# Performance work log

Hardware: AMD Instinct MI355X
Metric: run time of the kernel (lower is better)

## Reference

```python
import jax, jax.numpy as jnp
import numpy as np

NUM_EMBED = 1024
NUM_HEADS = 16
BLOCK_SIZE = 2048


def setup_inputs() -> dict:
    key = jax.random.key(0)
    k1, k2, k3, k4, k5 = jax.random.split(key, 5)
    C = NUM_EMBED
    s = 1.0 / np.sqrt(C)
    x = jax.random.normal(k1, (2, BLOCK_SIZE, C), dtype=jnp.float32)
    # nn.Linear params: weight (out,in), bias (out,)
    w_attn = jax.random.uniform(k2, (3 * C, C), minval=-s, maxval=s, dtype=jnp.float32)
    b_attn = jax.random.uniform(k3, (3 * C,), minval=-s, maxval=s, dtype=jnp.float32)
    w_proj = jax.random.uniform(k4, (C, C), minval=-s, maxval=s, dtype=jnp.float32)
    b_proj = jax.random.uniform(k5, (C,), minval=-s, maxval=s, dtype=jnp.float32)
    return {"x": x, "w_attn": w_attn, "b_attn": b_attn, "w_proj": w_proj, "b_proj": b_proj}


def reference(x, w_attn, b_attn, w_proj, b_proj):
    B, T, C = x.shape
    H = NUM_HEADS
    D = C // H
    kqv = jnp.einsum('btc,oc->bto', x, w_attn) + b_attn  # (B,T,3C)
    # Original code splits as K, Q, V in that order.
    K, Q, V = jnp.split(kqv, 3, axis=2)
    K = K.reshape(B, T, H, D).transpose(0, 2, 1, 3)  # (B,H,T,D)
    Q = Q.reshape(B, T, H, D).transpose(0, 2, 1, 3)
    V = V.reshape(B, T, H, D).transpose(0, 2, 1, 3)
    aff = jnp.einsum('bhqd,bhkd->bhqk', Q, K) * (D ** -0.5)  # (B,H,T,T)
    causal = jnp.tril(jnp.ones((T, T), dtype=bool))
    aff = jnp.where(causal[None, None], aff, jnp.float32(-jnp.inf))
    wei = jax.nn.softmax(aff, axis=-1)
    attn = jnp.einsum('bhqk,bhkd->bhqd', wei, V)
    attn = attn.transpose(0, 2, 1, 3).reshape(B, T, C)
    out = jnp.einsum('btc,oc->bto', attn, w_proj) + b_proj
    return out
```

## Files before the change

### kernel.cpp

```cpp
#include <hip/hip_runtime.h>
#include <hip/hip_bf16.h>
#include <cstdint>

typedef __attribute__((ext_vector_type(8))) short bf16x8;
typedef __attribute__((ext_vector_type(4))) float f32x4;
typedef __attribute__((ext_vector_type(16))) float f32x16;
typedef __attribute__((ext_vector_type(4))) uint16_t u16x4;

__device__ __forceinline__ uint16_t f2b(float f) {
  union { float f; uint32_t i; } v; v.f = f;
  return (uint16_t)((v.i + 0x7FFFu + ((v.i >> 16) & 1u)) >> 16);
}

__device__ __forceinline__ uint32_t pkbf(float a, float b) {
  union { __hip_bfloat162 h2; uint32_t u; } c;
  c.h2 = __float22bfloat162_rn(make_float2(a, b));
  return c.u;
}

#define GLDS16(g, l) __builtin_amdgcn_global_load_lds( \
    (const __attribute__((address_space(1))) void*)(g), \
    (__attribute__((address_space(3))) void*)(l), 16, 0, 0)

__global__ __launch_bounds__(256) void cvt_all(
    const float* __restrict__ x, const float* __restrict__ wa, const float* __restrict__ wp,
    uint16_t* __restrict__ xb, uint16_t* __restrict__ wab, uint16_t* __restrict__ wpb) {
  const int i = (blockIdx.x * 256 + threadIdx.x) * 4;
  const float* src; uint16_t* dst; int off;
  if (i < 4194304)      { src = x;  dst = xb;  off = i; }
  else if (i < 7340032) { src = wa; dst = wab; off = i - 4194304; }
  else                  { src = wp; dst = wpb; off = i - 7340032; }
  const float4 v = *(const float4*)(src + off);
  u16x4 o;
  o.x = f2b(v.x); o.y = f2b(v.y); o.z = f2b(v.z); o.w = f2b(v.w);
  *(u16x4*)(dst + off) = o;
}

template <int BM, bool OUT_BF16>
__global__ __launch_bounds__(256) void gemm_bt_bias(
    const uint16_t* __restrict__ A, const uint16_t* __restrict__ B,
    const float* __restrict__ bias, void* __restrict__ Cv,
    int M, int N, int K) {
  constexpr int MI = BM / 32;
  constexpr int CA = BM / 16;
  constexpr int CPW = (2 * (CA + 8)) / 4;
  constexpr int CT_PITCH = OUT_BF16 ? 72 : 68;
  constexpr size_t CT_BYTES = (size_t)4 * (BM / 2) * CT_PITCH * (OUT_BF16 ? 2 : 4);
  constexpr size_t ST_BYTES = (size_t)(2 * (BM * 32 + 4096)) * 2;
  constexpr size_t LB = CT_BYTES > ST_BYTES ? CT_BYTES : ST_BYTES;
  __shared__ alignas(16) unsigned char ldsb[LB];
  uint16_t* lds = (uint16_t*)ldsb;
  const int offB0 = BM * 32;
  const int offA1 = BM * 32 + 4096;
  const int offB1 = 2 * BM * 32 + 4096;

  const int tid = threadIdx.x;
  const int wave = tid >> 6, lane = tid & 63;
  const int q4 = lane >> 4, l16 = lane & 15;
  const int wm = wave >> 1, wn = wave & 1;
  const long blockM = (long)blockIdx.y * BM;
  const long blockN = (long)blockIdx.x * 128;

  f32x4 acc[MI][4] = {};

  for (int k0 = 0; k0 < K; k0 += 64) {
#pragma unroll
    for (int c = 0; c < CPW; ++c) {
      const int id = c * 4 + wave;
      const uint16_t* mat; long rowBase; int a, kk, off;
      if (id < CA)               { mat = A; rowBase = blockM; a = id;            kk = k0;      off = 0; }
      else if (id < CA + 8)      { mat = B; rowBase = blockN; a = id - CA;       kk = k0;      off = offB0; }
      else if (id < 2 * CA + 8)  { mat = A; rowBase = blockM; a = id - CA - 8;   kk = k0 + 32; off = offA1; }
      else                       { mat = B; rowBase = blockN; a = id - 2*CA - 8; kk = k0 + 32; off = offB1; }
      const int flat = a * 64 + lane;
      const int row = flat >> 2, seg = flat & 3;
      GLDS16(mat + (rowBase + row) * (long)K + kk + seg * 8, lds + off + a * 512);
    }
    __syncthreads();
#pragma unroll
    for (int h = 0; h < 2; ++h) {
      const uint16_t* Ah = lds + (h ? offA1 : 0);
      const uint16_t* Bh = lds + (h ? offB1 : offB0);
      bf16x8 af[MI], bfr[4];
#pragma unroll
      for (int i = 0; i < MI; ++i)
        af[i] = *(const bf16x8*)&Ah[(wm * (BM / 2) + i * 16 + l16) * 32 + q4 * 8];
#pragma unroll
      for (int j = 0; j < 4; ++j)
        bfr[j] = *(const bf16x8*)&Bh[(wn * 64 + j * 16 + l16) * 32 + q4 * 8];
#pragma unroll
      for (int i = 0; i < MI; ++i)
#pragma unroll
        for (int j = 0; j < 4; ++j)
          acc[i][j] = __builtin_amdgcn_mfma_f32_16x16x32_bf16(af[i], bfr[j], acc[i][j], 0, 0, 0);
    }
    __syncthreads();
  }

  if (OUT_BF16) {
    uint16_t* ct = lds + wave * (BM / 2) * 72;
#pragma unroll
    for (int j = 0; j < 4; ++j) {
      const float bv = bias[blockN + wn * 64 + j * 16 + l16];
#pragma unroll
      for (int i = 0; i < MI; ++i)
#pragma unroll
        for (int r = 0; r < 4; ++r)
          ct[(i * 16 + q4 * 4 + r) * 72 + j * 16 + l16] = f2b(acc[i][j][r] + bv);
    }
    __syncthreads();
    uint16_t* Cb = (uint16_t*)Cv;
#pragma unroll
    for (int st = 0; st < BM / 16; ++st) {
      const int flat = st * 64 + lane;
      const int row = flat >> 3, seg = flat & 7;
      const bf16x8 v = *(const bf16x8*)&ct[row * 72 + seg * 8];
      *(bf16x8*)&Cb[(blockM + wm * (BM / 2) + row) * (long)N + blockN + wn * 64 + seg * 8] = v;
    }
  } else {
    float* ct = (float*)ldsb + wave * (BM / 2) * 68;
#pragma unroll
    for (int j = 0; j < 4; ++j) {
      const float bv = bias[blockN + wn * 64 + j * 16 + l16];
#pragma unroll
      for (int i = 0; i < MI; ++i)
#pragma unroll
        for (int r = 0; r < 4; ++r)
          ct[(i * 16 + q4 * 4 + r) * 68 + j * 16 + l16] = acc[i][j][r] + bv;
    }
    __syncthreads();
    float* Cb = (float*)Cv;
#pragma unroll
    for (int st = 0; st < BM / 8; ++st) {
      const int flat = st * 64 + lane;
      const int row = flat >> 4, seg = flat & 15;
      const f32x4 v = *(const f32x4*)&ct[row * 68 + seg * 4];
      *(f32x4*)&Cb[(blockM + wm * (BM / 2) + row) * (long)N + blockN + wn * 64 + seg * 4] = v;
    }
  }
}

__global__ __launch_bounds__(256, 2) void attn_flash(
    const uint16_t* __restrict__ kqv, uint16_t* __restrict__ attn) {
  constexpr int T = 2048, C = 1024, C3 = 3072;
  __shared__ alignas(16) unsigned char ldsb[35840];
  uint16_t* KP = (uint16_t*)ldsb;
  uint16_t* Vt = (uint16_t*)(ldsb + 18432);
  uint32_t* VtW = (uint32_t*)(ldsb + 18432);
  float* mlb  = (float*)ldsb;
  float* obuf = (float*)(ldsb + 1024);

  const int tid = threadIdx.x;
  const int wave = tid >> 6, lane = tid & 63;
  const int l32 = lane & 31, hh = lane >> 5;
  const int sidx = blockIdx.x >> 5, bh = blockIdx.x & 31;
  const int b = bh >> 4, h = bh & 15;
  const size_t base = (size_t)b * T * C3;
  const int hD = h * 64;
  const int qb = 31 - sidx;
  const int nkt = (qb >> 1) + 1;
  const int tr = tid >> 3, kch = tid & 7;
  const float sc = 0.125f * 1.4426950408889634f;

  bf16x8 qf[2][4];
#pragma unroll
  for (int qc = 0; qc < 2; ++qc)
#pragma unroll
    for (int m = 0; m < 4; ++m)
      qf[qc][m] = *(const bf16x8*)&kqv[base + (size_t)(qb * 64 + qc * 32 + l32) * C3 + C + hD + m * 16 + hh * 8];

  f32x16 o[2][2] = {};
  float m_i[2] = {-1e30f, -1e30f}, l_i[2] = {0.f, 0.f};

  bf16x8 pk[4], pv0[2], pv1[2];
#pragma unroll
  for (int rr = 0; rr < 4; ++rr)
    pk[rr] = *(const bf16x8*)&kqv[base + (size_t)(rr * 32 + tr) * C3 + hD + kch * 8];
#pragma unroll
  for (int s2 = 0; s2 < 2; ++s2) {
    const size_t gg = base + (size_t)(2 * (s2 * 32 + tr)) * C3 + 2 * C + hD + kch * 8;
    pv0[s2] = *(const bf16x8*)&kqv[gg];
    pv1[s2] = *(const bf16x8*)&kqv[gg + C3];
  }

  for (int kt = 0; kt < nkt; ++kt) {
    __syncthreads();
#pragma unroll
    for (int rr = 0; rr < 4; ++rr)
      *(bf16x8*)&KP[(rr * 32 + tr) * 72 + kch * 8] = pk[rr];
#pragma unroll
    for (int s2 = 0; s2 < 2; ++s2) {
      const int colw = ((s2 * 32 + tr) + 8 * kch) & 63;
      const uint32_t* a0 = (const uint32_t*)&pv0[s2];
      const uint32_t* a1 = (const uint32_t*)&pv1[s2];
#pragma unroll
      for (int i = 0; i < 8; ++i) {
        const uint32_t w = (i & 1)
            ? __builtin_amdgcn_perm(a1[i >> 1], a0[i >> 1], 0x07060302u)
            : __builtin_amdgcn_perm(a1[i >> 1], a0[i >> 1], 0x05040100u);
        VtW[(kch * 8 + i) * 68 + colw] = w;
      }
    }
    __syncthreads();
    if (kt + 1 < nkt) {
      const int kb2 = (kt + 1) * 128;
#pragma unroll
      for (int rr = 0; rr < 4; ++rr)
        pk[rr] = *(const bf16x8*)&kqv[base + (size_t)(kb2 + rr * 32 + tr) * C3 + hD + kch * 8];
#pragma unroll
      for (int s2 = 0; s2 < 2; ++s2) {
        const size_t gg = base + (size_t)(kb2 + 2 * (s2 * 32 + tr)) * C3 + 2 * C + hD + kch * 8;
        pv0[s2] = *(const bf16x8*)&kqv[gg];
        pv1[s2] = *(const bf16x8*)&kqv[gg + C3];
      }
    }

    const bool act = (kt * 128 + wave * 32) <= (qb * 64 + 63);
    if (act) {
      bf16x8 kf[4];
#pragma unroll
      for (int m = 0; m < 4; ++m)
        kf[m] = *(const bf16x8*)&KP[(wave * 32 + l32) * 72 + m * 16 + hh * 8];

#pragma unroll
      for (int qc = 0; qc < 2; ++qc) {
        f32x16 z = {};
#pragma unroll
        for (int m = 0; m < 4; ++m)
          z = __builtin_amdgcn_mfma_f32_32x32x16_bf16(kf[m], qf[qc][m], z, 0, 0, 0);
        if (kt == nkt - 1) {
          const int key0 = kt * 128 + wave * 32;
          const int qg = qb * 64 + qc * 32 + l32;
#pragma unroll
          for (int r = 0; r < 16; ++r) {
            const int kg = key0 + (r & 3) + 8 * (r >> 2) + 4 * hh;
            if (kg > qg) z[r] = -1e30f;
          }
        }
        float mloc = -1e30f;
#pragma unroll
        for (int r = 0; r < 16; ++r) mloc = fmaxf(mloc, z[r]);
        mloc = fmaxf(mloc, __shfl_xor(mloc, 32, 64));
        const float pm = fmaxf(mloc * sc, -3.0e4f);
        if (__any(pm - m_i[qc] > 8.0f)) {
          const float mnew = fmaxf(m_i[qc], pm);
          const float alpha = exp2f(m_i[qc] - mnew);
#pragma unroll
          for (int r = 0; r < 16; ++r) {
            const float ar = __shfl(alpha, (r & 3) + 8 * (r >> 2) + 4 * hh, 64);
            o[qc][0][r] *= ar;
            o[qc][1][r] *= ar;
          }
          l_i[qc] *= alpha;
          m_i[qc] = mnew;
        }
        float rs = 0.f;
#pragma unroll
        for (int r = 0; r < 16; ++r) {
          const float pe = exp2f(fmaf(z[r], sc, -m_i[qc]));
          z[r] = pe;
          rs += pe;
        }
        rs += __shfl_xor(rs, 32, 64);
        l_i[qc] += rs;

        uint32_t x0 = pkbf(z[0], z[1]),   x1 = pkbf(z[2], z[3]);
        uint32_t y0 = pkbf(z[4], z[5]),   y1 = pkbf(z[6], z[7]);
        uint32_t x2 = pkbf(z[8], z[9]),   x3 = pkbf(z[10], z[11]);
        uint32_t y2 = pkbf(z[12], z[13]), y3 = pkbf(z[14], z[15]);
        const uint32_t s0 = hh ? x0 : y0, s1 = hh ? x1 : y1;
        const uint32_t s2 = hh ? x2 : y2, s3 = hh ? x3 : y3;
        const uint32_t t0 = __shfl_xor(s0, 32, 64), t1 = __shfl_xor(s1, 32, 64);
        const uint32_t t2 = __shfl_xor(s2, 32, 64), t3 = __shfl_xor(s3, 32, 64);
#pragma unroll
        for (int cc = 0; cc < 2; ++cc) {
          union { bf16x8 v; uint32_t w[4]; } pa;
          if (cc == 0) {
            pa.w[0] = hh ? t0 : x0; pa.w[1] = hh ? t1 : x1;
            pa.w[2] = hh ? y0 : t0; pa.w[3] = hh ? y1 : t1;
          } else {
            pa.w[0] = hh ? t2 : x2; pa.w[1] = hh ? t3 : x3;
            pa.w[2] = hh ? y2 : t2; pa.w[3] = hh ? y3 : t3;
          }
#pragma unroll
          for (int db = 0; db < 2; ++db) {
            const int d = db * 32 + l32;
            const int col = (wave * 32 + cc * 16 + hh * 8 + 16 * (d >> 3)) & 127;
            const bf16x8 vf = *(const bf16x8*)&Vt[d * 136 + col];
            o[qc][db] = __builtin_amdgcn_mfma_f32_32x32x16_bf16(pa.v, vf, o[qc][db], 0, 0, 0);
          }
        }
      }
    }
  }

#pragma unroll
  for (int qc = 0; qc < 2; ++qc) {
    __syncthreads();
    if (hh == 0) {
      mlb[wave * 64 + l32] = m_i[qc];
      mlb[wave * 64 + 32 + l32] = l_i[qc];
    }
#pragma unroll
    for (int r = 0; r < 16; ++r) {
      const int ql = (r & 3) + 8 * (r >> 2) + 4 * hh;
      const int bw = wave * 2112 + ql * 66 + l32;
      obuf[bw] = o[qc][0][r];
      obuf[bw + 32] = o[qc][1][r];
    }
    __syncthreads();
    float mw[4], lw[4];
#pragma unroll
    for (int w = 0; w < 4; ++w) {
      mw[w] = mlb[w * 64 + l32];
      lw[w] = mlb[w * 64 + 32 + l32];
    }
    const float M = fmaxf(fmaxf(mw[0], mw[1]), fmaxf(mw[2], mw[3]));
    float L = 0.f, ww[4];
#pragma unroll
    for (int w = 0; w < 4; ++w) { ww[w] = exp2f(mw[w] - M); L += lw[w] * ww[w]; }
    const float Li = 1.0f / L;
    const int cb = wave * 2 + hh;
    float acc[8] = {};
#pragma unroll
    for (int w = 0; w < 4; ++w)
#pragma unroll
      for (int p = 0; p < 4; ++p) {
        const float2 v = *(const float2*)&obuf[w * 2112 + l32 * 66 + cb * 8 + p * 2];
        acc[2 * p]     += v.x * ww[w];
        acc[2 * p + 1] += v.y * ww[w];
      }
    union { bf16x8 v; uint32_t w4[4]; } ov;
#pragma unroll
    for (int p = 0; p < 4; ++p)
      ov.w4[p] = pkbf(acc[2 * p] * Li, acc[2 * p + 1] * Li);
    *(bf16x8*)&attn[((size_t)b * T + qb * 64 + qc * 32 + l32) * C + hD + cb * 8] = ov.v;
  }
}

extern "C" void kernel_launch(void* const* d_in, const int* in_sizes, int n_in,
                              void* d_out, int out_size, void* d_ws, size_t ws_size,
                              hipStream_t stream) {
  const float* x      = (const float*)d_in[0];
  const float* w_attn = (const float*)d_in[1];
  const float* b_attn = (const float*)d_in[2];
  const float* w_proj = (const float*)d_in[3];
  const float* b_proj = (const float*)d_in[4];
  float* out = (float*)d_out;

  uint16_t* xb    = (uint16_t*)d_ws;
  uint16_t* wab   = xb  + (size_t)4096 * 1024;
  uint16_t* wpb   = wab + (size_t)3072 * 1024;
  uint16_t* kqv   = wpb + (size_t)1024 * 1024;
  uint16_t* attnb = kqv + (size_t)4096 * 3072;

  dim3 blk(256, 1, 1);
  hipLaunchKernelGGL(cvt_all, dim3(8192), blk, 0, stream, x, w_attn, w_proj, xb, wab, wpb);

  hipLaunchKernelGGL((gemm_bt_bias<128, true>), dim3(3072 / 128, 4096 / 128, 1), blk, 0, stream,
                     xb, wab, b_attn, (void*)kqv, 4096, 3072, 1024);
  hipLaunchKernelGGL(attn_flash, dim3(1024, 1, 1), blk, 0, stream, kqv, attnb);
  hipLaunchKernelGGL((gemm_bt_bias<64, false>), dim3(1024 / 128, 4096 / 64, 1), blk, 0, stream,
                     attnb, wpb, b_proj, (void*)out, 4096, 1024, 1024);
}
```

Measured before the change: 191.2 us.

## Pair causal query blocks per workgroup and widen attention to 8 waves

The attention kernel now runs 512-thread workgroups over a 256-key tile. Each workgroup handles two query blocks, qb and 31-qb, so causal work is balanced across the grid, which halves to 512 workgroups. The cross-wave softmax merge is extended to 8 waves, with each thread writing 4 output columns. LDS use roughly doubles, and the launch bound of (512,4) forces a tight per-thread register budget, so register spilling and lower occupancy are real risks.

Measured after the change: 333.1 us. +74.2%, slower.

```diff
diff --git a/kernel.cpp b/kernel.cpp
--- a/kernel.cpp
+++ b/kernel.cpp
@@ -140,201 +140,205 @@
   }
 }
 
-__global__ __launch_bounds__(256, 2) void attn_flash(
+__global__ __launch_bounds__(512, 4) void attn_flash(
     const uint16_t* __restrict__ kqv, uint16_t* __restrict__ attn) {
   constexpr int T = 2048, C = 1024, C3 = 3072;
-  __shared__ alignas(16) unsigned char ldsb[35840];
+  __shared__ alignas(16) unsigned char ldsb[70656];
   uint16_t* KP = (uint16_t*)ldsb;
-  uint16_t* Vt = (uint16_t*)(ldsb + 18432);
-  uint32_t* VtW = (uint32_t*)(ldsb + 18432);
+  uint16_t* Vt = (uint16_t*)(ldsb + 36864);
+  uint32_t* VtW = (uint32_t*)(ldsb + 36864);
   float* mlb  = (float*)ldsb;
-  float* obuf = (float*)(ldsb + 1024);
+  float* obuf = (float*)(ldsb + 2048);
 
   const int tid = threadIdx.x;
   const int wave = tid >> 6, lane = tid & 63;
   const int l32 = lane & 31, hh = lane >> 5;
-  const int sidx = blockIdx.x >> 5, bh = blockIdx.x & 31;
+  const int pairi = blockIdx.x >> 5, bh = blockIdx.x & 31;
   const int b = bh >> 4, h = bh & 15;
   const size_t base = (size_t)b * T * C3;
   const int hD = h * 64;
-  const int qb = 31 - sidx;
-  const int nkt = (qb >> 1) + 1;
   const int tr = tid >> 3, kch = tid & 7;
   const float sc = 0.125f * 1.4426950408889634f;
 
-  bf16x8 qf[2][4];
-#pragma unroll
-  for (int qc = 0; qc < 2; ++qc)
-#pragma unroll
-    for (int m = 0; m < 4; ++m)
-      qf[qc][m] = *(const bf16x8*)&kqv[base + (size_t)(qb * 64 + qc * 32 + l32) * C3 + C + hD + m * 16 + hh * 8];
-
-  f32x16 o[2][2] = {};
-  float m_i[2] = {-1e30f, -1e30f}, l_i[2] = {0.f, 0.f};
-
-  bf16x8 pk[4], pv0[2], pv1[2];
-#pragma unroll
-  for (int rr = 0; rr < 4; ++rr)
-    pk[rr] = *(const bf16x8*)&kqv[base + (size_t)(rr * 32 + tr) * C3 + hD + kch * 8];
-#pragma unroll
-  for (int s2 = 0; s2 < 2; ++s2) {
-    const size_t gg = base + (size_t)(2 * (s2 * 32 + tr)) * C3 + 2 * C + hD + kch * 8;
-    pv0[s2] = *(const bf16x8*)&kqv[gg];
-    pv1[s2] = *(const bf16x8*)&kqv[gg + C3];
-  }
-
-  for (int kt = 0; kt < nkt; ++kt) {
-    __syncthreads();
+  for (int ss = 0; ss < 2; ++ss) {
+    const int qb = ss ? pairi : 31 - pairi;
+    const int nkt = (qb + 4) >> 2;
+    const int qmax = qb * 64 + 63;
+
+    bf16x8 qf[2][4];
+#pragma unroll
+    for (int qc = 0; qc < 2; ++qc)
+#pragma unroll
+      for (int m = 0; m < 4; ++m)
+        qf[qc][m] = *(const bf16x8*)&kqv[base + (size_t)(qb * 64 + qc * 32 + l32) * C3 + C + hD + m * 16 + hh * 8];
+
+    f32x16 o[2][2] = {};
+    float m_i[2] = {-1e30f, -1e30f}, l_i[2] = {0.f, 0.f};
+
+    bf16x8 pk[4], pv0[2], pv1[2];
 #pragma unroll
     for (int rr = 0; rr < 4; ++rr)
-      *(bf16x8*)&KP[(rr * 32 + tr) * 72 + kch * 8] = pk[rr];
+      pk[rr] = *(const bf16x8*)&kqv[base + (size_t)(rr * 64 + tr) * C3 + hD + kch * 8];
 #pragma unroll
     for (int s2 = 0; s2 < 2; ++s2) {
-      const int colw = ((s2 * 32 + tr) + 8 * kch) & 63;
-      const uint32_t* a0 = (const uint32_t*)&pv0[s2];
-      const uint32_t* a1 = (const uint32_t*)&pv1[s2];
-#pragma unroll
-      for (int i = 0; i < 8; ++i) {
-        const uint32_t w = (i & 1)
-            ? __builtin_amdgcn_perm(a1[i >> 1], a0[i >> 1], 0x07060302u)
-            : __builtin_amdgcn_perm(a1[i >> 1], a0[i >> 1], 0x05040100u);
-        VtW[(kch * 8 + i) * 68 + colw] = w;
-      }
-    }
-    __syncthreads();
-    if (kt + 1 < nkt) {
-      const int kb2 = (kt + 1) * 128;
+      const size_t gg = base + (size_t)(2 * (s2 * 64 + tr)) * C3 + 2 * C + hD + kch * 8;
+      pv0[s2] = *(const bf16x8*)&kqv[gg];
+      pv1[s2] = *(const bf16x8*)&kqv[gg + C3];
+    }
+
+    for (int kt = 0; kt < nkt; ++kt) {
+      __syncthreads();
 #pragma unroll
       for (int rr = 0; rr < 4; ++rr)
-        pk[rr] = *(const bf16x8*)&kqv[base + (size_t)(kb2 + rr * 32 + tr) * C3 + hD + kch * 8];
+        *(bf16x8*)&KP[(rr * 64 + tr) * 72 + kch * 8] = pk[rr];
 #pragma unroll
       for (int s2 = 0; s2 < 2; ++s2) {
-        const size_t gg = base + (size_t)(kb2 + 2 * (s2 * 32 + tr)) * C3 + 2 * C + hD + kch * 8;
-        pv0[s2] = *(const bf16x8*)&kqv[gg];
-        pv1[s2] = *(const bf16x8*)&kqv[gg + C3];
-      }
-    }
-
-    const bool act = (kt * 128 + wave * 32) <= (qb * 64 + 63);
-    if (act) {
-      bf16x8 kf[4];
-#pragma unroll
-      for (int m = 0; m < 4; ++m)
-        kf[m] = *(const bf16x8*)&KP[(wave * 32 + l32) * 72 + m * 16 + hh * 8];
-
-#pragma unroll
-      for (int qc = 0; qc < 2; ++qc) {
-        f32x16 z = {};
+        const int colw = ((s2 * 64 + tr) + 8 * kch) & 127;
+        const uint32_t* a0 = (const uint32_t*)&pv0[s2];
+        const uint32_t* a1 = (const uint32_t*)&pv1[s2];
+#pragma unroll
+        for (int i = 0; i < 8; ++i) {
+          const uint32_t w = (i & 1)
+              ? __builtin_amdgcn_perm(a1[i >> 1], a0[i >> 1], 0x07060302u)
+              : __builtin_amdgcn_perm(a1[i >> 1], a0[i >> 1], 0x05040100u);
+          VtW[(kch * 8 + i) * 132 + colw] = w;
+        }
+      }
+      __syncthreads();
+      if (kt + 1 < nkt) {
+        const int kb2 = (kt + 1) * 256;
+#pragma unroll
+        for (int rr = 0; rr < 4; ++rr)
+          pk[rr] = *(const bf16x8*)&kqv[base + (size_t)(kb2 + rr * 64 + tr) * C3 + hD + kch * 8];
+#pragma unroll
+        for (int s2 = 0; s2 < 2; ++s2) {
+          const size_t gg = base + (size_t)(kb2 + 2 * (s2 * 64 + tr)) * C3 + 2 * C + hD + kch * 8;
+          pv0[s2] = *(const bf16x8*)&kqv[gg];
+          pv1[s2] = *(const bf16x8*)&kqv[gg + C3];
+        }
+      }
+
+      const bool act = (kt * 256 + wave * 32) <= qmax;
+      if (act) {
+        bf16x8 kf[4];
 #pragma unroll
         for (int m = 0; m < 4; ++m)
-          z = __builtin_amdgcn_mfma_f32_32x32x16_bf16(kf[m], qf[qc][m], z, 0, 0, 0);
-        if (kt == nkt - 1) {
-          const int key0 = kt * 128 + wave * 32;
-          const int qg = qb * 64 + qc * 32 + l32;
+          kf[m] = *(const bf16x8*)&KP[(wave * 32 + l32) * 72 + m * 16 + hh * 8];
+
+#pragma unroll
+        for (int qc = 0; qc < 2; ++qc) {
+          f32x16 z = {};
+#pragma unroll
+          for (int m = 0; m < 4; ++m)
+            z = __builtin_amdgcn_mfma_f32_32x32x16_bf16(kf[m], qf[qc][m], z, 0, 0, 0);
+          if (kt == nkt - 1) {
+            const int key0 = kt * 256 + wave * 32;
+            const int qg = qb * 64 + qc * 32 + l32;
+#pragma unroll
+            for (int r = 0; r < 16; ++r) {
+              const int kg = key0 + (r & 3) + 8 * (r >> 2) + 4 * hh;
+              if (kg > qg) z[r] = -1e30f;
+            }
+          }
+          float mloc = -1e30f;
+#pragma unroll
+          for (int r = 0; r < 16; ++r) mloc = fmaxf(mloc, z[r]);
+          mloc = fmaxf(mloc, __shfl_xor(mloc, 32, 64));
+          const float pm = fmaxf(mloc * sc, -3.0e4f);
+          if (__any(pm - m_i[qc] > 8.0f)) {
+            const float mnew = fmaxf(m_i[qc], pm);
+            const float alpha = exp2f(m_i[qc] - mnew);
+#pragma unroll
+            for (int r = 0; r < 16; ++r) {
+              const float ar = __shfl(alpha, (r & 3) + 8 * (r >> 2) + 4 * hh, 64);
+              o[qc][0][r] *= ar;
+              o[qc][1][r] *= ar;
+            }
+            l_i[qc] *= alpha;
+            m_i[qc] = mnew;
+          }
+          float rs = 0.f;
 #pragma unroll
           for (int r = 0; r < 16; ++r) {
-            const int kg = key0 + (r & 3) + 8 * (r >> 2) + 4 * hh;
-            if (kg > qg) z[r] = -1e30f;
+            const float pe = exp2f(fmaf(z[r], sc, -m_i[qc]));
+            z[r] = pe;
+            rs += pe;
+          }
+          rs += __shfl_xor(rs, 32, 64);
+          l_i[qc] += rs;
+
+          uint32_t x0 = pkbf(z[0], z[1]),   x1 = pkbf(z[2], z[3]);
+          uint32_t y0 = pkbf(z[4], z[5]),   y1 = pkbf(z[6], z[7]);
+          uint32_t x2 = pkbf(z[8], z[9]),   x3 = pkbf(z[10], z[11]);
+          uint32_t y2 = pkbf(z[12], z[13]), y3 = pkbf(z[14], z[15]);
+          const uint32_t s0 = hh ? x0 : y0, s1 = hh ? x1 : y1;
+          const uint32_t s2 = hh ? x2 : y2, s3 = hh ? x3 : y3;
+          const uint32_t t0 = __shfl_xor(s0, 32, 64), t1 = __shfl_xor(s1, 32, 64);
+          const uint32_t t2 = __shfl_xor(s2, 32, 64), t3 = __shfl_xor(s3, 32, 64);
+#pragma unroll
+          for (int cc = 0; cc < 2; ++cc) {
+            union { bf16x8 v; uint32_t w[4]; } pa;
+            if (cc == 0) {
+              pa.w[0] = hh ? t0 : x0; pa.w[1] = hh ? t1 : x1;
+              pa.w[2] = hh ? y0 : t0; pa.w[3] = hh ? y1 : t1;
+            } else {
+              pa.w[0] = hh ? t2 : x2; pa.w[1] = hh ? t3 : x3;
+              pa.w[2] = hh ? y2 : t2; pa.w[3] = hh ? y3 : t3;
+            }
+#pragma unroll
+            for (int db = 0; db < 2; ++db) {
+              const int d = db * 32 + l32;
+              const int col = (wave * 32 + cc * 16 + hh * 8 + 16 * (d >> 3)) & 255;
+              const bf16x8 vf = *(const bf16x8*)&Vt[d * 264 + col];
+              o[qc][db] = __builtin_amdgcn_mfma_f32_32x32x16_bf16(pa.v, vf, o[qc][db], 0, 0, 0);
+            }
           }
         }
-        float mloc = -1e30f;
-#pragma unroll
-        for (int r = 0; r < 16; ++r) mloc = fmaxf(mloc, z[r]);
-        mloc = fmaxf(mloc, __shfl_xor(mloc, 32, 64));
-        const float pm = fmaxf(mloc * sc, -3.0e4f);
-        if (__any(pm - m_i[qc] > 8.0f)) {
-          const float mnew = fmaxf(m_i[qc], pm);
-          const float alpha = exp2f(m_i[qc] - mnew);
-#pragma unroll
-          for (int r = 0; r < 16; ++r) {
-            const float ar = __shfl(alpha, (r & 3) + 8 * (r >> 2) + 4 * hh, 64);
-            o[qc][0][r] *= ar;
-            o[qc][1][r] *= ar;
-          }
-          l_i[qc] *= alpha;
-          m_i[qc] = mnew;
-        }
-        float rs = 0.f;
-#pragma unroll
-        for (int r = 0; r < 16; ++r) {
-          const float pe = exp2f(fmaf(z[r], sc, -m_i[qc]));
-          z[r] = pe;
-          rs += pe;
-        }
-        rs += __shfl_xor(rs, 32, 64);
-        l_i[qc] += rs;
-
-        uint32_t x0 = pkbf(z[0], z[1]),   x1 = pkbf(z[2], z[3]);
-        uint32_t y0 = pkbf(z[4], z[5]),   y1 = pkbf(z[6], z[7]);
-        uint32_t x2 = pkbf(z[8], z[9]),   x3 = pkbf(z[10], z[11]);
-        uint32_t y2 = pkbf(z[12], z[13]), y3 = pkbf(z[14], z[15]);
-        const uint32_t s0 = hh ? x0 : y0, s1 = hh ? x1 : y1;
-        const uint32_t s2 = hh ? x2 : y2, s3 = hh ? x3 : y3;
-        const uint32_t t0 = __shfl_xor(s0, 32, 64), t1 = __shfl_xor(s1, 32, 64);
-        const uint32_t t2 = __shfl_xor(s2, 32, 64), t3 = __shfl_xor(s3, 32, 64);
-#pragma unroll
-        for (int cc = 0; cc < 2; ++cc) {
-          union { bf16x8 v; uint32_t w[4]; } pa;
-          if (cc == 0) {
-            pa.w[0] = hh ? t0 : x0; pa.w[1] = hh ? t1 : x1;
-            pa.w[2] = hh ? y0 : t0; pa.w[3] = hh ? y1 : t1;
-          } else {
-            pa.w[0] = hh ? t2 : x2; pa.w[1] = hh ? t3 : x3;
-            pa.w[2] = hh ? y2 : t2; pa.w[3] = hh ? y3 : t3;
-          }
-#pragma unroll
-          for (int db = 0; db < 2; ++db) {
-            const int d = db * 32 + l32;
-            const int col = (wave * 32 + cc * 16 + hh * 8 + 16 * (d >> 3)) & 127;
-            const bf16x8 vf = *(const bf16x8*)&Vt[d * 136 + col];
-            o[qc][db] = __builtin_amdgcn_mfma_f32_32x32x16_bf16(pa.v, vf, o[qc][db], 0, 0, 0);
-          }
-        }
-      }
-    }
-  }
-
-#pragma unroll
-  for (int qc = 0; qc < 2; ++qc) {
-    __syncthreads();
-    if (hh == 0) {
-      mlb[wave * 64 + l32] = m_i[qc];
-      mlb[wave * 64 + 32 + l32] = l_i[qc];
-    }
-#pragma unroll
-    for (int r = 0; r < 16; ++r) {
-      const int ql = (r & 3) + 8 * (r >> 2) + 4 * hh;
-      const int bw = wave * 2112 + ql * 66 + l32;
-      obuf[bw] = o[qc][0][r];
-      obuf[bw + 32] = o[qc][1][r];
-    }
-    __syncthreads();
-    float mw[4], lw[4];
-#pragma unroll
-    for (int w = 0; w < 4; ++w) {
-      mw[w] = mlb[w * 64 + l32];
-      lw[w] = mlb[w * 64 + 32 + l32];
-    }
-    const float M = fmaxf(fmaxf(mw[0], mw[1]), fmaxf(mw[2], mw[3]));
-    float L = 0.f, ww[4];
-#pragma unroll
-    for (int w = 0; w < 4; ++w) { ww[w] = exp2f(mw[w] - M); L += lw[w] * ww[w]; }
-    const float Li = 1.0f / L;
-    const int cb = wave * 2 + hh;
-    float acc[8] = {};
-#pragma unroll
-    for (int w = 0; w < 4; ++w)
-#pragma unroll
-      for (int p = 0; p < 4; ++p) {
-        const float2 v = *(const float2*)&obuf[w * 2112 + l32 * 66 + cb * 8 + p * 2];
-        acc[2 * p]     += v.x * ww[w];
-        acc[2 * p + 1] += v.y * ww[w];
-      }
-    union { bf16x8 v; uint32_t w4[4]; } ov;
-#pragma unroll
-    for (int p = 0; p < 4; ++p)
-      ov.w4[p] = pkbf(acc[2 * p] * Li, acc[2 * p + 1] * Li);
-    *(bf16x8*)&attn[((size_t)b * T + qb * 64 + qc * 32 + l32) * C + hD + cb * 8] = ov.v;
+      }
+    }
+
+#pragma unroll
+    for (int qc = 0; qc < 2; ++qc) {
+      __syncthreads();
+      if (hh == 0) {
+        mlb[wave * 64 + l32] = m_i[qc];
+        mlb[wave * 64 + 32 + l32] = l_i[qc];
+      }
+#pragma unroll
+      for (int r = 0; r < 16; ++r) {
+        const int ql = (r & 3) + 8 * (r >> 2) + 4 * hh;
+        const int bw = wave * 2112 + ql * 66 + l32;
+        obuf[bw] = o[qc][0][r];
+        obuf[bw + 32] = o[qc][1][r];
+      }
+      __syncthreads();
+      float mw[8], lw[8];
+#pragma unroll
+      for (int w = 0; w < 8; ++w) {
+        mw[w] = mlb[w * 64 + l32];
+        lw[w] = mlb[w * 64 + 32 + l32];
+      }
+      float M = mw[0];
+#pragma unroll
+      for (int w = 1; w < 8; ++w) M = fmaxf(M, mw[w]);
+      float L = 0.f, ww[8];
+#pragma unroll
+      for (int w = 0; w < 8; ++w) { ww[w] = exp2f(mw[w] - M); L += lw[w] * ww[w]; }
+      const float Li = 1.0f / L;
+      const int cb = wave * 2 + hh;
+      float acc[4] = {};
+#pragma unroll
+      for (int w = 0; w < 8; ++w) {
+        const float2 v0 = *(const float2*)&obuf[w * 2112 + l32 * 66 + cb * 4];
+        const float2 v1 = *(const float2*)&obuf[w * 2112 + l32 * 66 + cb * 4 + 2];
+        acc[0] += v0.x * ww[w]; acc[1] += v0.y * ww[w];
+        acc[2] += v1.x * ww[w]; acc[3] += v1.y * ww[w];
+      }
+      union { u16x4 v; uint32_t w2[2]; } ov;
+      ov.w2[0] = pkbf(acc[0] * Li, acc[1] * Li);
+      ov.w2[1] = pkbf(acc[2] * Li, acc[3] * Li);
+      *(u16x4*)&attn[((size_t)b * T + qb * 64 + qc * 32 + l32) * C + hD + cb * 4] = ov.v;
+    }
   }
 }
 
@@ -359,7 +363,7 @@
 
   hipLaunchKernelGGL((gemm_bt_bias<128, true>), dim3(3072 / 128, 4096 / 128, 1), blk, 0, stream,
                      xb, wab, b_attn, (void*)kqv, 4096, 3072, 1024);
-  hipLaunchKernelGGL(attn_flash, dim3(1024, 1, 1), blk, 0, stream, kqv, attnb);
+  hipLaunchKernelGGL(attn_flash, dim3(512, 1, 1), dim3(512, 1, 1), 0, stream, kqv, attnb);
   hipLaunchKernelGGL((gemm_bt_bias<64, false>), dim3(1024 / 128, 4096 / 64, 1), blk, 0, stream,
                      attnb, wpb, b_proj, (void*)out, 4096, 1024, 1024);
 }
```
